# Kernel optimization log

Hardware: AMD Instinct MI355X
Metric: run time of the kernel (lower is better)

Reference implementation:

```python
import jax, jax.numpy as jnp
import numpy as np


def _conv_reflect(x, w, bias, dil, pad):
    # x: [N,3,H,W], w: [1,3,5,5] -> [N,1,H,W], reflect padding, dilated 5x5 conv
    xp = jnp.pad(x, ((0, 0), (0, 0), (pad, pad), (pad, pad)), mode='reflect')
    out = jax.lax.conv_general_dilated(
        xp, w, window_strides=(1, 1), padding='VALID',
        rhs_dilation=(dil, dil), dimension_numbers=('NCHW', 'OIHW', 'NCHW'))
    return out + bias[None, :, None, None]


def _triplets(x):
    # x: [B,T,H,W] -> [B,T,3,H,W] with (prev, cur, next), reflected at temporal ends
    T = x.shape[1]
    idx = jnp.arange(T)
    prev = jnp.where(idx == 0, 1, idx - 1)
    nxt = jnp.where(idx == T - 1, T - 2, idx + 1)
    return jnp.stack([x[:, prev], x, x[:, nxt]], axis=2)


def _denoise_block(x, w1, b1, w2, b2, w3, b3, a, b, c):
    # x: [B,T,H,W] -> [B,T,H,W]
    trip = _triplets(x)                      # [B,T,3,H,W]
    B, T, C, H, W = trip.shape
    xf = trip.reshape(B * T, C, H, W)
    o = (a * _conv_reflect(xf, w1, b1, 1, 2)
         + b * _conv_reflect(xf, w2, b2, 2, 4)
         + c * _conv_reflect(xf, w3, b3, 4, 8))
    return jnp.tanh(o).reshape(B, T, H, W)


def setup_inputs() -> dict:
    key = jax.random.key(0)
    ks = jax.random.split(key, 16)
    B, T, H, W = 4, 16, 512, 512
    inp = {'x': jax.random.normal(ks[0], (B, T, H, W), dtype=jnp.float32)}
    # conv weight init scale ~ kaiming-uniform-ish for fan_in = 3*5*5
    s = 1.0 / np.sqrt(3 * 5 * 5)
    i = 1
    for blk in (1, 2):
        for br in (1, 2, 3):
            inp[f'blk{blk}_w{br}'] = jax.random.uniform(ks[i], (1, 3, 5, 5), jnp.float32, -s, s); i += 1
            inp[f'blk{blk}_b{br}'] = jax.random.uniform(ks[i], (1,), jnp.float32, -s, s); i += 1
        inp[f'blk{blk}_a'] = jnp.float32(0.1)
        inp[f'blk{blk}_b'] = jnp.float32(0.1)
        inp[f'blk{blk}_c'] = jnp.float32(0.1)
    return inp


def reference(x,
              blk1_w1, blk1_b1, blk1_w2, blk1_b2, blk1_w3, blk1_b3,
              blk1_a, blk1_b, blk1_c,
              blk2_w1, blk2_b1, blk2_w2, blk2_b2, blk2_w3, blk2_b3,
              blk2_a, blk2_b, blk2_c):
    y = _denoise_block(x, blk1_w1, blk1_b1, blk1_w2, blk1_b2, blk1_w3, blk1_b3,
                       blk1_a, blk1_b, blk1_c)
    z = _denoise_block(y, blk2_w1, blk2_b1, blk2_w2, blk2_b2, blk2_w3, blk2_b3,
                       blk2_a, blk2_b, blk2_c)
    return z
```

## Files before the change

### kernel.cpp

```cpp
#include <hip/hip_runtime.h>
#include <hip/hip_fp16.h>

#define BB 4
#define TT 16
#define HH 512
#define WW 512
#define SP 528

#define BTILE 64
#define ROWB 160
#define PROWS 80
#define PLANE_STRIDE 13312
#define LDS_BYTES (3 * PLANE_STRIDE)

typedef _Float16 half8 __attribute__((ext_vector_type(8)));
typedef float f32x4 __attribute__((ext_vector_type(4)));

constexpr int kR[9] = {-8, -4, -2, -1, 0, 1, 2, 4, 8};

__device__ __forceinline__ int reflect_idx(int q, int n) {
    q = abs(q);
    if (q >= n) q = 2 * n - 2 - q;
    return q;
}

__device__ __forceinline__ void async_cp16(const __half* g, char* l) {
#if __has_builtin(__builtin_amdgcn_global_load_lds)
    __builtin_amdgcn_global_load_lds(
        (const __attribute__((address_space(1))) unsigned int*)g,
        (__attribute__((address_space(3))) unsigned int*)l, 16, 0, 0);
#else
    *reinterpret_cast<uint4*>(l) = *reinterpret_cast<const uint4*>(g);
#endif
}

__global__ void pack_bfrag(const float* __restrict__ w1, const float* __restrict__ b1,
                           const float* __restrict__ w2, const float* __restrict__ b2,
                           const float* __restrict__ w3, const float* __restrict__ b3,
                           const float* __restrict__ sa, const float* __restrict__ sb,
                           const float* __restrict__ sc_, __half* __restrict__ bfrag) {
    const int tid = threadIdx.x;
    float s[3] = {sa[0], sb[0], sc_[0]};
    const float* wp[3] = {w1, w2, w3};
    for (int idx = tid; idx < 27 * 64; idx += 256) {
        int mat = idx >> 6;
        int lane = idx & 63;
        int ch = mat / 9, ri = mat % 9;
        int r = kR[ri];
        int j = lane & 15, kg = lane >> 4;
        union { __half h[8]; uint4 u; } v;
#pragma unroll
        for (int e = 0; e < 8; ++e) {
            int k = kg * 8 + e;
            int c = k - 8 - j;
            float a = 0.f;
            if (c >= -8 && c <= 8) {
                for (int b = 0; b < 3; ++b) {
                    int d = 1 << b;
                    if (r % d == 0 && c % d == 0) {
                        int rd = r / d, cd = c / d;
                        if (rd >= -2 && rd <= 2 && cd >= -2 && cd <= 2)
                            a += s[b] * wp[b][ch * 25 + (rd + 2) * 5 + (cd + 2)];
                    }
                }
            }
            v.h[e] = __float2half(a);
        }
        *reinterpret_cast<uint4*>(bfrag + idx * 8) = v.u;
    }
    if (tid == 0)
        *reinterpret_cast<float*>(bfrag + 27 * 64 * 8) = s[0] * b1[0] + s[1] * b2[0] + s[2] * b3[0];
}

template <int PASS>
__global__ __launch_bounds__(256, 4) void conv_mfma(const void* __restrict__ xin,
                                                    void* __restrict__ outp,
                                                    const __half* __restrict__ bfrag) {
    __shared__ char lds[LDS_BYTES];

    const int bt = blockIdx.z;
    const int t  = bt % TT;
    const int h0 = blockIdx.y * BTILE;
    const int w0 = blockIdx.x * BTILE;
    const int tid = threadIdx.x;
    const int lane = tid & 63;
    const int wv = tid >> 6;

    const int tprev = (t == 0) ? 1 : t - 1;
    const int tnext = (t == TT - 1) ? TT - 2 : t + 1;
    const int bbase = (bt / TT) * TT;

    if constexpr (PASS == 1) {
        const float* x = (const float*)xin;
        const size_t fs = (size_t)HH * WW;
        const float* f0 = x + (size_t)(bbase + tprev) * fs;
        const float* f1 = x + (size_t)bt * fs;
        const float* f2 = x + (size_t)(bbase + tnext) * fs;
        for (int k2 = tid; k2 < 2400; k2 += 256) {
            int ch  = k2 / 800;
            int rem = k2 - ch * 800;
            int row = rem / 10;
            int c8  = rem - row * 10;
            const float* src = (ch == 0) ? f0 : (ch == 1) ? f1 : f2;
            int gh = reflect_idx(h0 - 8 + row, HH);
            int gb = w0 - 8 + c8 * 8;
            const float* rp = src + (size_t)gh * WW;
            union { __half h[8]; uint4 u; } cv;
            if (gb >= 0 && gb + 7 < WW) {
                const float4 v0 = *reinterpret_cast<const float4*>(rp + gb);
                const float4 v1 = *reinterpret_cast<const float4*>(rp + gb + 4);
                cv.h[0] = __float2half(v0.x); cv.h[1] = __float2half(v0.y);
                cv.h[2] = __float2half(v0.z); cv.h[3] = __float2half(v0.w);
                cv.h[4] = __float2half(v1.x); cv.h[5] = __float2half(v1.y);
                cv.h[6] = __float2half(v1.z); cv.h[7] = __float2half(v1.w);
            } else {
#pragma unroll
                for (int e = 0; e < 8; ++e)
                    cv.h[e] = __float2half(rp[reflect_idx(gb + e, WW)]);
            }
            *reinterpret_cast<uint4*>(lds + ch * PLANE_STRIDE + row * ROWB + c8 * 16) = cv.u;
        }
        __syncthreads();
    } else {
        const __half* y = (const __half*)xin;
        const size_t fsP = (size_t)HH * SP;
        const __half* f0 = y + (size_t)(bbase + tprev) * fsP;
        const __half* f1 = y + (size_t)bt * fsP;
        const __half* f2 = y + (size_t)(bbase + tnext) * fsP;
        for (int c = wv; c < 39; c += 4) {
            int plane = c / 13;
            int sub   = c - plane * 13;
            const __half* srcf = (plane == 0) ? f0 : (plane == 1) ? f1 : f2;
            int byt = sub * 1024 + lane * 16;
            if (byt < PROWS * ROWB) {
                int row  = byt / ROWB;
                int colh = (byt - row * ROWB) >> 1;
                int gh = reflect_idx(h0 - 8 + row, HH);
                const __half* g = srcf + (size_t)gh * SP + (w0 + colh);
                async_cp16(g, lds + plane * PLANE_STRIDE + byt);
            }
        }
        asm volatile("s_waitcnt vmcnt(0)" ::: "memory");
        __syncthreads();
    }

    const float bias = *reinterpret_cast<const float*>(bfrag + 27 * 64 * 8);
    f32x4 acc0 = {bias, bias, bias, bias};
    f32x4 acc1 = acc0, acc2 = acc0, acc3 = acc0;

    const int i16 = lane & 15;
    const int kg  = lane >> 4;
    const char* aB0 = lds + (16 * wv + i16) * ROWB + kg * 16;

#pragma unroll
    for (int ch = 0; ch < 3; ++ch) {
        const char* aB = aB0 + ch * PLANE_STRIDE;
        const __half* bp = bfrag + (size_t)ch * 9 * 512 + lane * 8;
        half8 bf[9];
#pragma unroll
        for (int ri = 0; ri < 9; ++ri)
            bf[ri] = *reinterpret_cast<const half8*>(bp + ri * 512);
#pragma unroll
        for (int ri = 0; ri < 9; ++ri) {
            const char* ar = aB + (kR[ri] + 8) * ROWB;
            half8 a0 = *reinterpret_cast<const half8*>(ar);
            half8 a1 = *reinterpret_cast<const half8*>(ar + 32);
            half8 a2 = *reinterpret_cast<const half8*>(ar + 64);
            half8 a3 = *reinterpret_cast<const half8*>(ar + 96);
            __builtin_amdgcn_s_setprio(1);
            acc0 = __builtin_amdgcn_mfma_f32_16x16x32_f16(a0, bf[ri], acc0, 0, 0, 0);
            acc1 = __builtin_amdgcn_mfma_f32_16x16x32_f16(a1, bf[ri], acc1, 0, 0, 0);
            acc2 = __builtin_amdgcn_mfma_f32_16x16x32_f16(a2, bf[ri], acc2, 0, 0, 0);
            acc3 = __builtin_amdgcn_mfma_f32_16x16x32_f16(a3, bf[ri], acc3, 0, 0, 0);
            __builtin_amdgcn_s_setprio(0);
        }
    }

    if constexpr (PASS == 1) {
        __half* yp = (__half*)outp + (size_t)bt * HH * SP;
#pragma unroll
        for (int sc = 0; sc < 4; ++sc) {
            f32x4 a = (sc == 0) ? acc0 : (sc == 1) ? acc1 : (sc == 2) ? acc2 : acc3;
            const int wcol = w0 + sc * 16 + i16;
#pragma unroll
            for (int v2 = 0; v2 < 4; ++v2) {
                float z = a[v2];
                float e = __expf(2.0f * z);
                z = 1.0f - 2.0f / (e + 1.0f);
                __half hz = __float2half(z);
                __half* rb = yp + (size_t)(h0 + 16 * wv + kg * 4 + v2) * SP;
                rb[8 + wcol] = hz;
                if (wcol >= 1 && wcol <= 8)          rb[8 - wcol] = hz;
                else if (wcol >= 503 && wcol <= 510) rb[1030 - wcol] = hz;
            }
        }
    } else {
        float* dst = (float*)outp + (size_t)bt * HH * WW
                   + (size_t)(h0 + 16 * wv + kg * 4) * WW + (w0 + i16);
#pragma unroll
        for (int sc = 0; sc < 4; ++sc) {
            f32x4 a = (sc == 0) ? acc0 : (sc == 1) ? acc1 : (sc == 2) ? acc2 : acc3;
#pragma unroll
            for (int v2 = 0; v2 < 4; ++v2) {
                float z = a[v2];
                float e = __expf(2.0f * z);
                dst[(size_t)v2 * WW + sc * 16] = 1.0f - 2.0f / (e + 1.0f);
            }
        }
    }
}

extern "C" void kernel_launch(void* const* d_in, const int* in_sizes, int n_in,
                              void* d_out, int out_size, void* d_ws, size_t ws_size,
                              hipStream_t stream) {
    const float* x = (const float*)d_in[0];
    char* ws = (char*)d_ws;
    __half* bf1  = (__half*)ws;
    __half* bf2  = (__half*)(ws + 32768);
    __half* ypad = (__half*)(ws + 65536);

    pack_bfrag<<<1, 256, 0, stream>>>((const float*)d_in[1], (const float*)d_in[2],
                                      (const float*)d_in[3], (const float*)d_in[4],
                                      (const float*)d_in[5], (const float*)d_in[6],
                                      (const float*)d_in[7], (const float*)d_in[8],
                                      (const float*)d_in[9], bf1);
    pack_bfrag<<<1, 256, 0, stream>>>((const float*)d_in[10], (const float*)d_in[11],
                                      (const float*)d_in[12], (const float*)d_in[13],
                                      (const float*)d_in[14], (const float*)d_in[15],
                                      (const float*)d_in[16], (const float*)d_in[17],
                                      (const float*)d_in[18], bf2);

    dim3 grid(WW / BTILE, HH / BTILE, BB * TT);
    conv_mfma<1><<<grid, 256, 0, stream>>>(x, ypad, bf1);
    conv_mfma<2><<<grid, 256, 0, stream>>>(ypad, d_out, bf2);
}
```

Before: 175.1 us.

## Double-buffer per-channel LDS staging to overlap loads with MFMA compute

The conv kernel now stages one input plane at a time into a two-slot LDS ring and issues the load for the next temporal channel before computing the current one. This is meant to hide global-load latency behind the MFMA work and to cut LDS use from three planes to two. The launch-bounds target rises from 4 to 5 blocks per CU so the smaller LDS footprint can buy more occupancy. The cost is extra barriers per channel and a tighter register budget, which could cause spills.

```diff
diff --git a/kernel.cpp b/kernel.cpp
--- a/kernel.cpp
+++ b/kernel.cpp
@@ -10,8 +10,9 @@
 #define BTILE 64
 #define ROWB 160
 #define PROWS 80
+#define PLANE_BYTES (PROWS * ROWB)
 #define PLANE_STRIDE 13312
-#define LDS_BYTES (3 * PLANE_STRIDE)
+#define LDS_BYTES (2 * PLANE_STRIDE)
 
 typedef _Float16 half8 __attribute__((ext_vector_type(8)));
 typedef float f32x4 __attribute__((ext_vector_type(4)));
@@ -42,7 +43,7 @@
     const int tid = threadIdx.x;
     float s[3] = {sa[0], sb[0], sc_[0]};
     const float* wp[3] = {w1, w2, w3};
-    for (int idx = tid; idx < 27 * 64; idx += 256) {
+    for (int idx = tid; idx < 27 * 64; idx += blockDim.x) {
         int mat = idx >> 6;
         int lane = idx & 63;
         int ch = mat / 9, ri = mat % 9;
@@ -73,7 +74,7 @@
 }
 
 template <int PASS>
-__global__ __launch_bounds__(256, 4) void conv_mfma(const void* __restrict__ xin,
+__global__ __launch_bounds__(256, 5) void conv_mfma(const void* __restrict__ xin,
                                                     void* __restrict__ outp,
                                                     const __half* __restrict__ bfrag) {
     __shared__ char lds[LDS_BYTES];
@@ -90,59 +91,59 @@
     const int tnext = (t == TT - 1) ? TT - 2 : t + 1;
     const int bbase = (bt / TT) * TT;
 
+    const void* fsrc[3];
     if constexpr (PASS == 1) {
         const float* x = (const float*)xin;
         const size_t fs = (size_t)HH * WW;
-        const float* f0 = x + (size_t)(bbase + tprev) * fs;
-        const float* f1 = x + (size_t)bt * fs;
-        const float* f2 = x + (size_t)(bbase + tnext) * fs;
-        for (int k2 = tid; k2 < 2400; k2 += 256) {
-            int ch  = k2 / 800;
-            int rem = k2 - ch * 800;
-            int row = rem / 10;
-            int c8  = rem - row * 10;
-            const float* src = (ch == 0) ? f0 : (ch == 1) ? f1 : f2;
-            int gh = reflect_idx(h0 - 8 + row, HH);
-            int gb = w0 - 8 + c8 * 8;
-            const float* rp = src + (size_t)gh * WW;
-            union { __half h[8]; uint4 u; } cv;
-            if (gb >= 0 && gb + 7 < WW) {
-                const float4 v0 = *reinterpret_cast<const float4*>(rp + gb);
-                const float4 v1 = *reinterpret_cast<const float4*>(rp + gb + 4);
-                cv.h[0] = __float2half(v0.x); cv.h[1] = __float2half(v0.y);
-                cv.h[2] = __float2half(v0.z); cv.h[3] = __float2half(v0.w);
-                cv.h[4] = __float2half(v1.x); cv.h[5] = __float2half(v1.y);
-                cv.h[6] = __float2half(v1.z); cv.h[7] = __float2half(v1.w);
-            } else {
-#pragma unroll
-                for (int e = 0; e < 8; ++e)
-                    cv.h[e] = __float2half(rp[reflect_idx(gb + e, WW)]);
-            }
-            *reinterpret_cast<uint4*>(lds + ch * PLANE_STRIDE + row * ROWB + c8 * 16) = cv.u;
-        }
-        __syncthreads();
+        fsrc[0] = x + (size_t)(bbase + tprev) * fs;
+        fsrc[1] = x + (size_t)bt * fs;
+        fsrc[2] = x + (size_t)(bbase + tnext) * fs;
     } else {
         const __half* y = (const __half*)xin;
         const size_t fsP = (size_t)HH * SP;
-        const __half* f0 = y + (size_t)(bbase + tprev) * fsP;
-        const __half* f1 = y + (size_t)bt * fsP;
-        const __half* f2 = y + (size_t)(bbase + tnext) * fsP;
-        for (int c = wv; c < 39; c += 4) {
-            int plane = c / 13;
-            int sub   = c - plane * 13;
-            const __half* srcf = (plane == 0) ? f0 : (plane == 1) ? f1 : f2;
-            int byt = sub * 1024 + lane * 16;
-            if (byt < PROWS * ROWB) {
-                int row  = byt / ROWB;
-                int colh = (byt - row * ROWB) >> 1;
+        fsrc[0] = y + (size_t)(bbase + tprev) * fsP;
+        fsrc[1] = y + (size_t)bt * fsP;
+        fsrc[2] = y + (size_t)(bbase + tnext) * fsP;
+    }
+
+    auto STAGE = [&](int ch, char* buf) {
+        if constexpr (PASS == 1) {
+            const float* src = (const float*)fsrc[ch];
+            for (int k2 = tid; k2 < PROWS * 10; k2 += 256) {
+                int row = k2 / 10;
+                int c8  = k2 - row * 10;
                 int gh = reflect_idx(h0 - 8 + row, HH);
-                const __half* g = srcf + (size_t)gh * SP + (w0 + colh);
-                async_cp16(g, lds + plane * PLANE_STRIDE + byt);
-            }
-        }
-        asm volatile("s_waitcnt vmcnt(0)" ::: "memory");
-        __syncthreads();
-    }
+                int gb = w0 - 8 + c8 * 8;
+                const float* rp = src + (size_t)gh * WW;
+                union { __half h[8]; uint4 u; } cv;
+                if (gb >= 0 && gb + 7 < WW) {
+                    const float4 v0 = *reinterpret_cast<const float4*>(rp + gb);
+                    const float4 v1 = *reinterpret_cast<const float4*>(rp + gb + 4);
+                    cv.h[0] = __float2half(v0.x); cv.h[1] = __float2half(v0.y);
+                    cv.h[2] = __float2half(v0.z); cv.h[3] = __float2half(v0.w);
+                    cv.h[4] = __float2half(v1.x); cv.h[5] = __float2half(v1.y);
+                    cv.h[6] = __float2half(v1.z); cv.h[7] = __float2half(v1.w);
+                } else {
+#pragma unroll
+                    for (int e = 0; e < 8; ++e)
+                        cv.h[e] = __float2half(rp[reflect_idx(gb + e, WW)]);
+                }
+                *reinterpret_cast<uint4*>(buf + row * ROWB + c8 * 16) = cv.u;
+            }
+        } else {
+            const __half* src = (const __half*)fsrc[ch];
+            for (int c = wv; c < 13; c += 4) {
+                int byt = c * 1024 + lane * 16;
+                if (byt < PLANE_BYTES) {
+                    int row  = byt / ROWB;
+                    int colh = (byt - row * ROWB) >> 1;
+                    int gh = reflect_idx(h0 - 8 + row, HH);
+                    const __half* g = src + (size_t)gh * SP + (w0 + colh);
+                    async_cp16(g, buf + byt);
+                }
+            }
+        }
+    };
 
     const float bias = *reinterpret_cast<const float*>(bfrag + 27 * 64 * 8);
     f32x4 acc0 = {bias, bias, bias, bias};
@@ -150,16 +151,15 @@
 
     const int i16 = lane & 15;
     const int kg  = lane >> 4;
-    const char* aB0 = lds + (16 * wv + i16) * ROWB + kg * 16;
-
-#pragma unroll
-    for (int ch = 0; ch < 3; ++ch) {
-        const char* aB = aB0 + ch * PLANE_STRIDE;
+    const int aoff = (16 * wv + i16) * ROWB + kg * 16;
+
+    auto COMPUTE = [&](int ch, const char* buf) {
         const __half* bp = bfrag + (size_t)ch * 9 * 512 + lane * 8;
         half8 bf[9];
 #pragma unroll
         for (int ri = 0; ri < 9; ++ri)
             bf[ri] = *reinterpret_cast<const half8*>(bp + ri * 512);
+        const char* aB = buf + aoff;
 #pragma unroll
         for (int ri = 0; ri < 9; ++ri) {
             const char* ar = aB + (kR[ri] + 8) * ROWB;
@@ -174,6 +174,16 @@
             acc3 = __builtin_amdgcn_mfma_f32_16x16x32_f16(a3, bf[ri], acc3, 0, 0, 0);
             __builtin_amdgcn_s_setprio(0);
         }
+    };
+
+    STAGE(0, lds);
+#pragma unroll 1
+    for (int ch = 0; ch < 3; ++ch) {
+        if constexpr (PASS == 2)
+            asm volatile("s_waitcnt vmcnt(0)" ::: "memory");
+        __syncthreads();
+        if (ch < 2) STAGE(ch + 1, lds + ((ch + 1) & 1) * PLANE_STRIDE);
+        COMPUTE(ch, lds + (ch & 1) * PLANE_STRIDE);
     }
 
     if constexpr (PASS == 1) {
```

Result: no change. 175.9 us (+0.4%).
